# Performance work log

Measured on AMD Instinct MI355X. Metric: run time of the kernel, lower is better.

The kernel has to match this reference:

```python
import jax, jax.numpy as jnp
import numpy as np
import math

H = 128
W = 128
N = 2048
DIM = 768
TWO_PI = 2.0 * math.pi
ALPHA_MIN = 1.0 / 255.0


def setup_inputs() -> dict:
    key = jax.random.key(0)
    ks = jax.random.split(key, 6)
    # _xyz = atanh(2*(rand-0.5)); clip uniform away from endpoints to avoid inf
    u = jax.random.uniform(ks[0], (N, 2), minval=1e-4, maxval=1.0 - 1e-4)
    xyz = jnp.arctanh(2.0 * (u - 0.5))
    scaling = jax.random.uniform(ks[1], (N, 2))
    rotation = jax.random.uniform(ks[2], (N, 1))
    features = jax.random.uniform(ks[3], (N, 3))
    opacity = jnp.ones((N, 1), jnp.float32)
    w_up = jax.random.normal(ks[4], (DIM, 3), jnp.float32) * 0.05
    b_up = jnp.zeros((DIM,), jnp.float32)
    x = jax.random.normal(ks[5], (1, DIM, H, W), jnp.float32)
    return {"x": x, "xyz": xyz, "scaling": scaling, "rotation": rotation,
            "features": features, "opacity": opacity, "w_up": w_up, "b_up": b_up}


def _forward(xyz, scaling, rotation, features, opacity, w_up, b_up):
    # activations (get_xyz / get_scaling / get_rotation)
    means = jnp.tanh(xyz)                                   # [N,2] in (-1,1)
    s = jnp.abs(scaling + 0.5)                              # [N,2]
    theta = jax.nn.sigmoid(rotation[:, 0]) * TWO_PI         # [N]
    c, sn = jnp.cos(theta), jnp.sin(theta)
    # M = R(theta) @ diag(s); cov2d = M M^T
    a = c * s[:, 0]; b = -sn * s[:, 1]
    d = sn * s[:, 0]; e = c * s[:, 1]
    cov_xx = a * a + b * b
    cov_xy = a * d + b * e
    cov_yy = d * d + e * e
    det = cov_xx * cov_yy - cov_xy * cov_xy
    # conic = inverse covariance (A, B, C)
    A = cov_yy / det; B = -cov_xy / det; C = cov_xx / det   # [N]
    # project [-1,1] -> pixel centers
    gx = 0.5 * (means[:, 0] + 1.0) * W                      # [N]
    gy = 0.5 * (means[:, 1] + 1.0) * H
    px = jnp.arange(W, dtype=jnp.float32) + 0.5
    py = jnp.arange(H, dtype=jnp.float32) + 0.5
    PX, PY = jnp.meshgrid(px, py)                           # [H,W], PX varies along W
    dx = gx[None, :] - PX.reshape(-1)[:, None]              # [P,N], P=H*W
    dy = gy[None, :] - PY.reshape(-1)[:, None]
    sigma = 0.5 * (A * dx * dx + C * dy * dy) + B * dx * dy # [P,N]
    alpha = jnp.minimum(0.999, opacity[:, 0][None, :] * jnp.exp(-sigma))
    alpha = jnp.where((sigma < 0.0) | (alpha < ALPHA_MIN), 0.0, alpha)
    # summation rasterizer: per-pixel weighted sum of colors
    img = jnp.clip(alpha @ features, 0.0, 1.0)              # [P,3]
    feat = img @ w_up.T + b_up                              # [P,DIM]
    return feat.T.reshape(1, DIM, H, W)


def reference(x, xyz, scaling, rotation, features, opacity, w_up, b_up):
    del x  # only its channel dim (== DIM) shapes the output in the original
    return _forward(xyz, scaling, rotation, features, opacity, w_up, b_up)
```

## Files before the change

kernel.cpp:

```cpp
#include <hip/hip_runtime.h>
#include <math.h>

#define HH 128
#define WW 128
#define NG 2048
#define DIMV 768
#define PIX (HH * WW)
#define A_MIN (1.0f / 255.0f)
#define TW 16
#define TH 4
#define TWO_PI 6.28318530717958647692f

__global__ __launch_bounds__(256) void raster_kernel(
    const float* __restrict__ xyz, const float* __restrict__ scaling,
    const float* __restrict__ rotation, const float* __restrict__ features,
    const float* __restrict__ opacity, float* __restrict__ img)
{
    __shared__ float4 sP0[NG];
    __shared__ float4 sP1[NG];
    __shared__ float2 sP2[NG];
    __shared__ int s_cnt;
    __shared__ int s_list[NG];
    __shared__ float s_red[4 * 64 * 3];

    int tid = threadIdx.x;
    int bx = blockIdx.x & 7, by = blockIdx.x >> 3;
    int px0 = bx * TW, py0 = by * TH;

    if (tid == 0) s_cnt = 0;

    for (int g = tid; g < NG; g += 256) {
        float2 xz = ((const float2*)xyz)[g];
        float e2x = __expf(2.0f * xz.x);
        float e2y = 2.0f * __expf(2.0f * xz.y);
        float gx = (e2x / (e2x + 1.0f)) * (float)WW;
        float gy = (e2y / (e2y + 2.0f)) * (float)HH;
        float2 sc = ((const float2*)scaling)[g];
        float s0 = fabsf(sc.x + 0.5f);
        float s1 = fabsf(sc.y + 0.5f);
        float th = TWO_PI / (1.0f + __expf(-rotation[g]));
        float sn = __sinf(th), cs = __cosf(th);
        float a = cs * s0, b = -sn * s1, d = sn * s0, e = cs * s1;
        float cxx = a * a + b * b;
        float cxy = a * d + b * e;
        float cyy = d * d + e * e;
        float inv = 1.0f / (cxx * cyy - cxy * cxy);
        float op = opacity[g];
        float L = __logf(255.0f * op);
        float r2 = (L > 0.0f) ? 2.0f * L * (cxx + cyy) * 1.0002f + 1e-3f : -1.0f;
        sP0[g] = make_float4(0.5f * cyy * inv, -cxy * inv, 0.5f * cxx * inv, op);
        sP1[g] = make_float4(gx, gy, features[3 * g + 0], features[3 * g + 1]);
        sP2[g] = make_float2(features[3 * g + 2], r2);
    }
    __syncthreads();

    {
        float x0 = px0 + 0.5f, x1 = px0 + TW - 0.5f;
        float y0 = py0 + 0.5f, y1 = py0 + TH - 0.5f;
        for (int g = tid; g < NG; g += 256) {
            float4 c1 = sP1[g];
            float2 c2 = sP2[g];
            float ddx = fmaxf(fmaxf(x0 - c1.x, c1.x - x1), 0.0f);
            float ddy = fmaxf(fmaxf(y0 - c1.y, c1.y - y1), 0.0f);
            if (ddx * ddx + ddy * ddy <= c2.y) {
                int pos = atomicAdd(&s_cnt, 1);
                s_list[pos] = g;
            }
        }
    }
    __syncthreads();
    int cnt = s_cnt;

    int lane = tid & 63, wv = tid >> 6;
    float pxf = px0 + (lane & 15) + 0.5f;
    float pyf = py0 + (lane >> 4) + 0.5f;

    float ar = 0.0f, ag = 0.0f, ab = 0.0f;
    for (int k = wv; k < cnt; k += 4) {
        int g = __builtin_amdgcn_readfirstlane(s_list[k]);
        float4 a0 = sP0[g];
        float4 a1 = sP1[g];
        float2 a2 = sP2[g];
        float dx = a1.x - pxf, dy = a1.y - pyf;
        float sig = fmaf(a0.y * dx, dy, fmaf(a0.x * dx, dx, a0.z * dy * dy));
        float al = fminf(0.999f, a0.w * __expf(-sig));
        al = (sig < 0.0f || al < A_MIN) ? 0.0f : al;
        ar = fmaf(al, a1.z, ar);
        ag = fmaf(al, a1.w, ag);
        ab = fmaf(al, a2.x, ab);
    }
    s_red[(wv * 64 + lane) * 3 + 0] = ar;
    s_red[(wv * 64 + lane) * 3 + 1] = ag;
    s_red[(wv * 64 + lane) * 3 + 2] = ab;
    __syncthreads();

    if (tid < 64) {
        float sr = 0.0f, sg = 0.0f, sb = 0.0f;
        #pragma unroll
        for (int w = 0; w < 4; ++w) {
            sr += s_red[(w * 64 + tid) * 3 + 0];
            sg += s_red[(w * 64 + tid) * 3 + 1];
            sb += s_red[(w * 64 + tid) * 3 + 2];
        }
        int p = (py0 + (tid >> 4)) * WW + px0 + (tid & 15);
        img[p]           = fminf(1.0f, fmaxf(0.0f, sr));
        img[PIX + p]     = fminf(1.0f, fmaxf(0.0f, sg));
        img[2 * PIX + p] = fminf(1.0f, fmaxf(0.0f, sb));
    }
}

__global__ __launch_bounds__(256) void project_kernel(
    const float* __restrict__ img, const float* __restrict__ w_up,
    const float* __restrict__ b_up, float* __restrict__ out)
{
    int grp = blockIdx.x >> 4;
    int seg = blockIdx.x & 15;
    int p = seg * 1024 + threadIdx.x * 4;
    float4 r = *(const float4*)(img + p);
    float4 g = *(const float4*)(img + PIX + p);
    float4 b = *(const float4*)(img + 2 * PIX + p);
    int d0 = grp * 4;
    #pragma unroll
    for (int i = 0; i < 4; ++i) {
        int d = d0 + i;
        float w0 = w_up[3 * d + 0], w1 = w_up[3 * d + 1], w2 = w_up[3 * d + 2];
        float bb = b_up[d];
        float4 v;
        v.x = fmaf(w0, r.x, fmaf(w1, g.x, fmaf(w2, b.x, bb)));
        v.y = fmaf(w0, r.y, fmaf(w1, g.y, fmaf(w2, b.y, bb)));
        v.z = fmaf(w0, r.z, fmaf(w1, g.z, fmaf(w2, b.z, bb)));
        v.w = fmaf(w0, r.w, fmaf(w1, g.w, fmaf(w2, b.w, bb)));
        *(float4*)(out + (size_t)d * PIX + p) = v;
    }
}

extern "C" void kernel_launch(void* const* d_in, const int* in_sizes, int n_in,
                              void* d_out, int out_size, void* d_ws, size_t ws_size,
                              hipStream_t stream)
{
    const float* xyz      = (const float*)d_in[1];
    const float* scaling  = (const float*)d_in[2];
    const float* rotation = (const float*)d_in[3];
    const float* features = (const float*)d_in[4];
    const float* opacity  = (const float*)d_in[5];
    const float* w_up     = (const float*)d_in[6];
    const float* b_up     = (const float*)d_in[7];
    float* out = (float*)d_out;
    float* img = (float*)d_ws;

    raster_kernel<<<256, 256, 0, stream>>>(xyz, scaling, rotation, features,
                                           opacity, img);
    project_kernel<<<(DIMV / 4) * 16, 256, 0, stream>>>(img, w_up, b_up, out);
}
```

Baseline: 114.3 us.

## Use smaller raster tiles with per-tile culling and compacted splat storage

Raster tiles shrink from 16x4 to 8x2 pixels, so the grid grows to 1024 blocks. Each block now culls Gaussians with a cheaper rotation-invariant bound and computes the full conic only for survivors, storing them compactly (capped at 768). The 16 pixels are split across 16 lane groups that each take a strided slice of the splat list, followed by a 16-way reduction. This trades redundant per-block preprocessing of all 2048 Gaussians for finer culling and more parallelism. Any overflow beyond 768 splats per tile is silently dropped.

```diff
diff --git a/kernel.cpp b/kernel.cpp
--- a/kernel.cpp
+++ b/kernel.cpp
@@ -7,80 +7,81 @@
 #define DIMV 768
 #define PIX (HH * WW)
 #define A_MIN (1.0f / 255.0f)
-#define TW 16
-#define TH 4
+#define TPX 8
+#define TPY 2
+#define MAXS 768
 #define TWO_PI 6.28318530717958647692f
 
-__global__ __launch_bounds__(256) void raster_kernel(
+__global__ __launch_bounds__(256, 4) void raster_kernel(
     const float* __restrict__ xyz, const float* __restrict__ scaling,
     const float* __restrict__ rotation, const float* __restrict__ features,
     const float* __restrict__ opacity, float* __restrict__ img)
 {
-    __shared__ float4 sP0[NG];
-    __shared__ float4 sP1[NG];
-    __shared__ float2 sP2[NG];
-    __shared__ int s_cnt;
-    __shared__ int s_list[NG];
-    __shared__ float s_red[4 * 64 * 3];
+    __shared__ float4 sQ0[MAXS];
+    __shared__ float4 sQ1[MAXS];
+    __shared__ float2 sQ2[MAXS];
+    __shared__ float  s_red[16 * 16 * 3];
+    __shared__ int    s_cnt;
 
     int tid = threadIdx.x;
-    int bx = blockIdx.x & 7, by = blockIdx.x >> 3;
-    int px0 = bx * TW, py0 = by * TH;
+    int px0 = (blockIdx.x & 15) * TPX;
+    int py0 = (blockIdx.x >> 4) * TPY;
 
     if (tid == 0) s_cnt = 0;
-
-    for (int g = tid; g < NG; g += 256) {
-        float2 xz = ((const float2*)xyz)[g];
-        float e2x = __expf(2.0f * xz.x);
-        float e2y = 2.0f * __expf(2.0f * xz.y);
-        float gx = (e2x / (e2x + 1.0f)) * (float)WW;
-        float gy = (e2y / (e2y + 2.0f)) * (float)HH;
-        float2 sc = ((const float2*)scaling)[g];
-        float s0 = fabsf(sc.x + 0.5f);
-        float s1 = fabsf(sc.y + 0.5f);
-        float th = TWO_PI / (1.0f + __expf(-rotation[g]));
-        float sn = __sinf(th), cs = __cosf(th);
-        float a = cs * s0, b = -sn * s1, d = sn * s0, e = cs * s1;
-        float cxx = a * a + b * b;
-        float cxy = a * d + b * e;
-        float cyy = d * d + e * e;
-        float inv = 1.0f / (cxx * cyy - cxy * cxy);
-        float op = opacity[g];
-        float L = __logf(255.0f * op);
-        float r2 = (L > 0.0f) ? 2.0f * L * (cxx + cyy) * 1.0002f + 1e-3f : -1.0f;
-        sP0[g] = make_float4(0.5f * cyy * inv, -cxy * inv, 0.5f * cxx * inv, op);
-        sP1[g] = make_float4(gx, gy, features[3 * g + 0], features[3 * g + 1]);
-        sP2[g] = make_float2(features[3 * g + 2], r2);
-    }
     __syncthreads();
 
     {
-        float x0 = px0 + 0.5f, x1 = px0 + TW - 0.5f;
-        float y0 = py0 + 0.5f, y1 = py0 + TH - 0.5f;
+        float x0 = px0 + 0.5f, x1 = px0 + TPX - 0.5f;
+        float y0 = py0 + 0.5f, y1 = py0 + TPY - 0.5f;
         for (int g = tid; g < NG; g += 256) {
-            float4 c1 = sP1[g];
-            float2 c2 = sP2[g];
-            float ddx = fmaxf(fmaxf(x0 - c1.x, c1.x - x1), 0.0f);
-            float ddy = fmaxf(fmaxf(y0 - c1.y, c1.y - y1), 0.0f);
-            if (ddx * ddx + ddy * ddy <= c2.y) {
+            float2 xz = ((const float2*)xyz)[g];
+            float2 sc = ((const float2*)scaling)[g];
+            float rt = rotation[g];
+            float op = opacity[g];
+            float e2x = __expf(2.0f * xz.x);
+            float gx = (e2x / (e2x + 1.0f)) * (float)WW;
+            float e2y = __expf(2.0f * xz.y);
+            float gy = (e2y / (e2y + 1.0f)) * (float)HH;
+            float s0 = fabsf(sc.x + 0.5f);
+            float s1 = fabsf(sc.y + 0.5f);
+            float tr = s0 * s0 + s1 * s1;
+            float L = __logf(255.0f * op);
+            float r2 = (L > 0.0f) ? 2.0f * L * tr * 1.0002f + 1e-3f : -1.0f;
+            float ddx = fmaxf(fmaxf(x0 - gx, gx - x1), 0.0f);
+            float ddy = fmaxf(fmaxf(y0 - gy, gy - y1), 0.0f);
+            if (ddx * ddx + ddy * ddy <= r2) {
                 int pos = atomicAdd(&s_cnt, 1);
-                s_list[pos] = g;
+                if (pos < MAXS) {
+                    float th = TWO_PI / (1.0f + __expf(-rt));
+                    float sn = __sinf(th), cs = __cosf(th);
+                    float a = cs * s0, b = -sn * s1, d = sn * s0, e = cs * s1;
+                    float cxx = a * a + b * b;
+                    float cxy = a * d + b * e;
+                    float cyy = d * d + e * e;
+                    float inv = 1.0f / (cxx * cyy - cxy * cxy);
+                    sQ0[pos] = make_float4(0.5f * cyy * inv, -cxy * inv,
+                                           0.5f * cxx * inv, op);
+                    sQ1[pos] = make_float4(gx, gy, features[3 * g + 0],
+                                           features[3 * g + 1]);
+                    sQ2[pos] = make_float2(features[3 * g + 2], 0.0f);
+                }
             }
         }
     }
     __syncthreads();
-    int cnt = s_cnt;
+    int cnt = min(s_cnt, MAXS);
 
     int lane = tid & 63, wv = tid >> 6;
-    float pxf = px0 + (lane & 15) + 0.5f;
-    float pyf = py0 + (lane >> 4) + 0.5f;
+    int px = lane & 15;
+    int ks = wv * 4 + (lane >> 4);
+    float pxf = px0 + (px & 7) + 0.5f;
+    float pyf = py0 + (px >> 3) + 0.5f;
 
     float ar = 0.0f, ag = 0.0f, ab = 0.0f;
-    for (int k = wv; k < cnt; k += 4) {
-        int g = __builtin_amdgcn_readfirstlane(s_list[k]);
-        float4 a0 = sP0[g];
-        float4 a1 = sP1[g];
-        float2 a2 = sP2[g];
+    for (int k = ks; k < cnt; k += 16) {
+        float4 a0 = sQ0[k];
+        float4 a1 = sQ1[k];
+        float2 a2 = sQ2[k];
         float dx = a1.x - pxf, dy = a1.y - pyf;
         float sig = fmaf(a0.y * dx, dy, fmaf(a0.x * dx, dx, a0.z * dy * dy));
         float al = fminf(0.999f, a0.w * __expf(-sig));
@@ -89,20 +90,22 @@
         ag = fmaf(al, a1.w, ag);
         ab = fmaf(al, a2.x, ab);
     }
-    s_red[(wv * 64 + lane) * 3 + 0] = ar;
-    s_red[(wv * 64 + lane) * 3 + 1] = ag;
-    s_red[(wv * 64 + lane) * 3 + 2] = ab;
+    int ri = (ks * 16 + px) * 3;
+    s_red[ri + 0] = ar;
+    s_red[ri + 1] = ag;
+    s_red[ri + 2] = ab;
     __syncthreads();
 
-    if (tid < 64) {
+    if (tid < 16) {
         float sr = 0.0f, sg = 0.0f, sb = 0.0f;
         #pragma unroll
-        for (int w = 0; w < 4; ++w) {
-            sr += s_red[(w * 64 + tid) * 3 + 0];
-            sg += s_red[(w * 64 + tid) * 3 + 1];
-            sb += s_red[(w * 64 + tid) * 3 + 2];
+        for (int j = 0; j < 16; ++j) {
+            int b = (j * 16 + tid) * 3;
+            sr += s_red[b + 0];
+            sg += s_red[b + 1];
+            sb += s_red[b + 2];
         }
-        int p = (py0 + (tid >> 4)) * WW + px0 + (tid & 15);
+        int p = (py0 + (tid >> 3)) * WW + px0 + (tid & 7);
         img[p]           = fminf(1.0f, fmaxf(0.0f, sr));
         img[PIX + p]     = fminf(1.0f, fmaxf(0.0f, sg));
         img[2 * PIX + p] = fminf(1.0f, fmaxf(0.0f, sb));
@@ -148,7 +151,7 @@
     float* out = (float*)d_out;
     float* img = (float*)d_ws;
 
-    raster_kernel<<<256, 256, 0, stream>>>(xyz, scaling, rotation, features,
-                                           opacity, img);
+    raster_kernel<<<(WW / TPX) * (HH / TPY), 256, 0, stream>>>(
+        xyz, scaling, rotation, features, opacity, img);
     project_kernel<<<(DIMV / 4) * 16, 256, 0, stream>>>(img, w_up, b_up, out);
 }
```

New measurement: 114.3 us. About the same (+0.0%).
